# Optimization experiments

Measured on AMD Instinct MI355X. Metric: run time of the kernel, lower is better.

Reference implementation:

```python
import jax, jax.numpy as jnp
import numpy as np

H = 128          # hidden_size
GRID = 4         # grid_dim
CELL = 0.5       # cell_size
PRED_LEN = 12
EMB = H // 4     # social pooling embed dim = 32


def setup_inputs() -> dict:
    key = jax.random.key(0)
    ks = jax.random.split(key, 13)
    B, N, T = 16384, 64, 8
    s = 0.05
    return {
        "obs": jax.random.normal(ks[0], (B, T, 2), jnp.float32),
        "neighbors": jax.random.normal(ks[1], (B, N, T, 2), jnp.float32),
        "embed_table": jax.random.normal(ks[2], (GRID * GRID + 1, EMB), jnp.float32) * s,
        "W_in": jax.random.normal(ks[3], (H, 2), jnp.float32) * s,
        "b_in": jax.random.normal(ks[4], (H,), jnp.float32) * s,
        "W_sp": jax.random.normal(ks[5], (H, EMB), jnp.float32) * s,
        "b_sp": jax.random.normal(ks[6], (H,), jnp.float32) * s,
        "W_ih": jax.random.normal(ks[7], (4 * H, 2 * H), jnp.float32) * s,
        "W_hh": jax.random.normal(ks[8], (4 * H, H), jnp.float32) * s,
        "b_ih": jax.random.normal(ks[9], (4 * H,), jnp.float32) * s,
        "b_hh": jax.random.normal(ks[10], (4 * H,), jnp.float32) * s,
        "W_out": jax.random.normal(ks[11], (2, H), jnp.float32) * s,
        "b_out": jax.random.normal(ks[12], (2,), jnp.float32) * s,
    }


def reference(obs, neighbors, embed_table, W_in, b_in, W_sp, b_sp,
              W_ih, W_hh, b_ih, b_hh, W_out, b_out):
    B = obs.shape[0]
    half = GRID // 2

    def pool(rel):  # rel: [B, N, 2] -> [B, EMB]
        idx = jnp.clip(jnp.floor(rel / CELL).astype(jnp.int32), -half, half - 1) + half
        # after clamp+shift, idx in [0, GRID-1], so index is always valid (matches torch path)
        flat = idx[..., 0] * GRID + idx[..., 1]  # [B, N]
        return embed_table[flat].sum(axis=1)     # sum-pool over neighbors

    def lstm(h, c, x):  # torch LSTMCell gate order: i, f, g, o
        gates = x @ W_ih.T + b_ih + h @ W_hh.T + b_hh  # [B, 4H]
        i, f, g, o = jnp.split(gates, 4, axis=-1)
        c2 = jax.nn.sigmoid(f) * c + jax.nn.sigmoid(i) * jnp.tanh(g)
        h2 = jax.nn.sigmoid(o) * jnp.tanh(c2)
        return h2, c2

    def obs_step(carry, xs):
        h, c = carry
        o_t, nb_t = xs  # [B,2], [B,N,2]
        agent = o_t @ W_in.T + b_in                        # [B,H]
        social = pool(nb_t - o_t[:, None, :]) @ W_sp.T + b_sp  # [B,H]
        h, c = lstm(h, c, jnp.concatenate([agent, social], axis=-1))
        return (h, c), None

    h0 = jnp.zeros((B, H), obs.dtype)
    c0 = jnp.zeros((B, H), obs.dtype)
    obs_tf = jnp.swapaxes(obs, 0, 1)          # [T,B,2]
    nb_tf = jnp.moveaxis(neighbors, 2, 0)     # [T,B,N,2]
    (h, c), _ = jax.lax.scan(obs_step, (h0, c0), (obs_tf, nb_tf))

    def pred_step(carry, _):
        h, c, prev = carry
        agent = prev @ W_in.T + b_in
        x = jnp.concatenate([agent, jnp.zeros_like(agent)], axis=-1)
        h, c = lstm(h, c, x)
        disp = h @ W_out.T + b_out  # [B,2]
        return (h, c, disp), disp

    prev0 = jnp.zeros((B, 2), obs.dtype)
    _, fut = jax.lax.scan(pred_step, (h, c, prev0), None, length=PRED_LEN)
    return jnp.swapaxes(fut, 0, 1)  # [B, PRED_LEN, 2]
```

## Files before the change

kernel.cpp:

```cpp
#include <hip/hip_runtime.h>
#include <math.h>

typedef _Float16 f16;
typedef f16 f16x8 __attribute__((ext_vector_type(8)));
typedef float f32x4 __attribute__((ext_vector_type(4)));

#define Bsz   16384
#define Tobs  8
#define PREDL 12
#define MR    32

__device__ __forceinline__ float fast_sigm(float x) {
  float e = __builtin_amdgcn_exp2f(-1.44269504f * x);
  return __builtin_amdgcn_rcpf(1.f + e);
}
__device__ __forceinline__ float fast_tanh(float x) {
  float e = __builtin_amdgcn_exp2f(2.88539008f * x);
  return 1.f - 2.f * __builtin_amdgcn_rcpf(1.f + e);
}

#define AB(buf, kt, mt, lane, j) (((((buf)*4 + (kt))*2 + (mt))*64 + (lane))*8 + (j))
#define CA(t, mt, lane, j) ((((t)*2 + (mt))*64 + (lane))*8 + (j))

#define WF(ktw, w, nt, lane) ((size_t)((((ktw)*8 + (w))*4 + (nt))*64 + (lane)) * 8)

__global__ __launch_bounds__(64) void pack_all(
    const float* __restrict__ W_ih, const float* __restrict__ W_hh,
    const float* __restrict__ W_in, const float* __restrict__ W_sp,
    const float* __restrict__ table,
    const float* __restrict__ b_in, const float* __restrict__ b_sp,
    const float* __restrict__ b_ih, const float* __restrict__ b_hh,
    const float* __restrict__ W_out, const float* __restrict__ b_out,
    f16* __restrict__ Wfrag, float* __restrict__ biasO,
    float* __restrict__ biasP, float* __restrict__ biasPE) {
  const int blk = blockIdx.x;
  const int nt = blk >> 7, w = (blk >> 4) & 7, l = blk & 15;
  const int jo = nt * 128 + w * 16 + l;
  const int m = threadIdx.x;
  __shared__ float st[256];
  __shared__ float wspPS[32];
  __shared__ float cellsS[16];

  float a0 = W_ih[jo * 256 + m],        a1 = W_ih[jo * 256 + 64 + m];
  float s0 = W_ih[jo * 256 + 128 + m],  s1 = W_ih[jo * 256 + 192 + m];
  float hh0 = W_hh[jo * 128 + m],       hh1 = W_hh[jo * 128 + 64 + m];
  float bi0 = b_in[m], bi1 = b_in[64 + m];
  float bs0 = b_sp[m], bs1 = b_sp[64 + m];
  float wi00 = W_in[m * 2 + 0],        wi01 = W_in[m * 2 + 1];
  float wi10 = W_in[(64 + m) * 2 + 0], wi11 = W_in[(64 + m) * 2 + 1];
  float wo00 = W_out[m],       wo01 = W_out[64 + m];
  float wo10 = W_out[128 + m], wo11 = W_out[192 + m];

  auto red = [](float v) {
#pragma unroll
    for (int s = 1; s < 64; s <<= 1) v += __shfl_xor(v, s);
    return v;
  };

#pragma unroll 4
  for (int e = 0; e < 32; ++e) {
    float wp = red(s0 * W_sp[m * 32 + e] + s1 * W_sp[(64 + m) * 32 + e]);
    if (m == e) wspPS[e] = wp;
  }
  __syncthreads();
  if (m < 16) {
    float s = 0.f;
#pragma unroll
    for (int e = 0; e < 32; ++e) s += table[m * 32 + e] * wspPS[e];
    cellsS[m] = s;
  }

  float wio0 = red(a0 * wi00 + a1 * wi10);
  float wio1 = red(a0 * wi01 + a1 * wi11);
  float dotA = red(a0 * bi0 + a1 * bi1);
  float dotS = red(s0 * bs0 + s1 * bs1);

  st[m] = hh0;
  st[64 + m] = hh1;
  st[128 + m] = hh0 + wio0 * wo00 + wio1 * wo10;
  st[192 + m] = hh1 + wio0 * wo01 + wio1 * wo11;
  __syncthreads();

  if (m < 32) {
    int u = m & 15, kt = u >> 2, q = u & 3;
    int which = m >> 4;
    int ktw = which ? kt + 5 : kt;
    f16x8 v;
#pragma unroll
    for (int j = 0; j < 8; ++j) v[j] = (f16)st[which * 128 + kt * 32 + q * 8 + j];
    *(f16x8*)(Wfrag + WF(ktw, w, nt, q * 16 + l)) = v;
  } else if (m < 36) {
    int q = m - 32;
    f16x8 v;
#pragma unroll
    for (int j = 0; j < 8; ++j) {
      int kk = q * 8 + j;
      float x = (kk < 16) ? cellsS[kk] : (kk == 16 ? wio0 : (kk == 17 ? wio1 : 0.f));
      v[j] = (f16)x;
    }
    *(f16x8*)(Wfrag + WF(4, w, nt, q * 16 + l)) = v;
  } else if (m == 36) {
    int col = w * 64 + nt * 16 + l;
    float base = b_ih[jo] + b_hh[jo];
    biasO[col] = base + dotA + dotS;
    float bp = base + dotA;
    biasP[col] = bp;
    biasPE[col] = bp + wio0 * b_out[0] + wio1 * b_out[1];
  }
}

__global__ __launch_bounds__(512, 2) void social_lstm_main(
    const float* __restrict__ obs, const float* __restrict__ nb,
    const f16* __restrict__ Wfrag, const float* __restrict__ biasO,
    const float* __restrict__ biasP, const float* __restrict__ biasPE,
    const float* __restrict__ W_out, const float* __restrict__ b_out,
    float* __restrict__ out) {
  __shared__ __align__(16) f16 Abuf[2 * 4 * 2 * 64 * 8];
  __shared__ __align__(16) f16 cntA[8 * 2 * 64 * 8];

  const int tid = threadIdx.x;
  const int w = tid >> 6, ln = tid & 63;
  const int q = ln >> 4, l = ln & 15;
  const int b0 = blockIdx.x * MR;

  for (int i = tid; i < 2048; i += 512) ((uint32_t*)Abuf)[i] = 0u;
  for (int i = tid; i < 4096; i += 512) ((uint32_t*)cntA)[i] = 0u;
  __syncthreads();

  {
    const int g = ln >> 4, lg = ln & 15;
    const int r = w * 4 + g;
    const float4* orow = (const float4*)(obs + (size_t)(b0 + r) * 16);
    float4 O0 = orow[0], O1 = orow[1], O2 = orow[2], O3 = orow[3];
    float ox[8] = {O0.x, O0.z, O1.x, O1.z, O2.x, O2.z, O3.x, O3.z};
    float oy[8] = {O0.y, O0.w, O1.y, O1.w, O2.y, O2.w, O3.y, O3.w};
    unsigned long long h[8] = {0ull, 0ull, 0ull, 0ull, 0ull, 0ull, 0ull, 0ull};
#pragma unroll
    for (int jt = 0; jt < 4; ++jt) {
      const float4* tr =
          (const float4*)(nb + ((size_t)(b0 + r) * 64 + (lg + 16 * jt)) * 16);
      float4 N0 = tr[0], N1 = tr[1], N2 = tr[2], N3 = tr[3];
      float nx[8] = {N0.x, N0.z, N1.x, N1.z, N2.x, N2.z, N3.x, N3.z};
      float ny[8] = {N0.y, N0.w, N1.y, N1.w, N2.y, N2.w, N3.y, N3.w};
#pragma unroll
      for (int t = 0; t < 8; ++t) {
        float rx = nx[t] - ox[t], ry = ny[t] - oy[t];
        int ix = (int)floorf(rx + rx);
        int iy = (int)floorf(ry + ry);
        ix = min(max(ix, -2), 1);
        iy = min(max(iy, -2), 1);
        int flat = (ix + 2) * 4 + (iy + 2);
        h[t] += 1ull << (flat * 4);
      }
    }
    auto shx = [](unsigned long long x, int msk) {
      unsigned lo = __shfl_xor((unsigned)x, msk);
      unsigned hi = __shfl_xor((unsigned)(x >> 32), msk);
      return ((unsigned long long)hi << 32) | lo;
    };
#pragma unroll
    for (int t = 0; t < 8; ++t) {
      unsigned long long v = h[t];
      v += shx(v, 1);
      unsigned long long e0 = v & 0x0F0F0F0F0F0F0F0Full;
      unsigned long long e1 = (v >> 4) & 0x0F0F0F0F0F0F0F0Full;
      e0 += shx(e0, 2); e1 += shx(e1, 2);
      e0 += shx(e0, 4); e1 += shx(e1, 4);
      e0 += shx(e0, 8); e1 += shx(e1, 8);
      unsigned long long wsel = (lg & 1) ? e1 : e0;
      unsigned cnt = (unsigned)(wsel >> ((lg >> 1) * 8)) & 0xFFu;
      cntA[CA(t, r >> 4, (lg >> 3) * 16 + (r & 15), lg & 7)] = (f16)(float)cnt;
    }
    int rr = tid >> 4, tt = (tid >> 1) & 7, comp = tid & 1;
    float xv = obs[(size_t)(b0 + rr) * 16 + tt * 2 + comp];
    cntA[CA(tt, rr >> 4, 2 * 16 + (rr & 15), comp)] = (f16)xv;
  }
  __builtin_amdgcn_sched_barrier(0);

  f16x8 Bh[4][4];
#pragma unroll
  for (int kt = 0; kt < 4; ++kt)
#pragma unroll
    for (int nt = 0; nt < 4; ++nt)
      Bh[kt][nt] = *(const f16x8*)(Wfrag + WF(kt, w, nt, ln));
  f16x8 Bx[4];
#pragma unroll
  for (int nt = 0; nt < 4; ++nt) Bx[nt] = *(const f16x8*)(Wfrag + WF(4, w, nt, ln));

  float creg[8];
#pragma unroll
  for (int i = 0; i < 8; ++i) creg[i] = 0.f;

  float bOr[4], bPr[4];
#pragma unroll
  for (int g2 = 0; g2 < 4; ++g2) {
    bOr[g2] = biasO[w * 64 + g2 * 16 + l];
    bPr[g2] = biasP[w * 64 + g2 * 16 + l];
  }

  const int hc = w * 16 + l;
  const int aw_kt = hc >> 5, aw_quad = (hc >> 3) & 3, aw_j = l & 7;

  f32x4 acc[2][4];

  auto acc_init = [&](const float* bq) {
#pragma unroll
    for (int mt = 0; mt < 2; ++mt)
#pragma unroll
      for (int nt = 0; nt < 4; ++nt)
        acc[mt][nt] = (f32x4){bq[nt], bq[nt], bq[nt], bq[nt]};
  };

  auto gemm_h = [&](int rb) {
#pragma unroll
    for (int kt = 0; kt < 4; ++kt) {
      f16x8 Af[2];
#pragma unroll
      for (int mt = 0; mt < 2; ++mt) Af[mt] = *(const f16x8*)(&Abuf[AB(rb, kt, mt, ln, 0)]);
#pragma unroll
      for (int mt = 0; mt < 2; ++mt)
#pragma unroll
        for (int nt = 0; nt < 4; ++nt)
          acc[mt][nt] =
              __builtin_amdgcn_mfma_f32_16x16x32_f16(Af[mt], Bh[kt][nt], acc[mt][nt], 0, 0, 0);
    }
  };

  auto epilogue = [&](int wbuf) {
#pragma unroll
    for (int mt = 0; mt < 2; ++mt) {
#pragma unroll
      for (int reg = 0; reg < 4; ++reg) {
        float p0 = acc[mt][0][reg];
        float p1 = acc[mt][1][reg];
        float p2 = acc[mt][2][reg];
        float p3 = acc[mt][3][reg];
        float iv = fast_sigm(p0), fv = fast_sigm(p1);
        float gv = fast_tanh(p2), ov = fast_sigm(p3);
        int ci = mt * 4 + reg;
        float c2 = fv * creg[ci] + iv * gv;
        creg[ci] = c2;
        float hv = ov * fast_tanh(c2);
        Abuf[AB(wbuf, aw_kt, mt, (q * 4 + reg) + 16 * aw_quad, aw_j)] = (f16)hv;
      }
    }
  };

#pragma unroll
  for (int t = 0; t < Tobs; ++t) {
    const int rb = t & 1, wb = rb ^ 1;
    __syncthreads();
    f16x8 Ax[2];
#pragma unroll
    for (int mt = 0; mt < 2; ++mt) Ax[mt] = *(const f16x8*)(&cntA[CA(t, mt, ln, 0)]);
    acc_init(bOr);
#pragma unroll
    for (int mt = 0; mt < 2; ++mt)
#pragma unroll
      for (int nt = 0; nt < 4; ++nt)
        acc[mt][nt] = __builtin_amdgcn_mfma_f32_16x16x32_f16(Ax[mt], Bx[nt], acc[mt][nt], 0, 0, 0);
    gemm_h(rb);
    epilogue(wb);
  }

  {
    const int rb = Tobs & 1, wb = rb ^ 1;
    __syncthreads();
    acc_init(bPr);
    gemm_h(rb);
    epilogue(wb);
  }

#pragma unroll
  for (int kt = 0; kt < 4; ++kt)
#pragma unroll
    for (int nt = 0; nt < 4; ++nt)
      Bh[kt][nt] = *(const f16x8*)(Wfrag + WF(kt + 5, w, nt, ln));
  float bEr[4];
#pragma unroll
  for (int g2 = 0; g2 < 4; ++g2) bEr[g2] = biasPE[w * 64 + g2 * 16 + l];

  const int d_oi = tid >> 3, d_seg = tid & 7;
  const int d_row = d_oi >> 1, d_jj = d_oi & 1;
  const int d_kt = d_seg >> 1, d_q0 = (d_seg & 1) * 2;
  float wor[16];
  {
    const float4* wp = (const float4*)(W_out + d_jj * 128 + d_seg * 16);
#pragma unroll
    for (int u = 0; u < 4; ++u) {
      float4 v = wp[u];
      wor[4 * u] = v.x; wor[4 * u + 1] = v.y; wor[4 * u + 2] = v.z; wor[4 * u + 3] = v.w;
    }
  }
  const float d_bo = b_out[d_jj];

  auto disp_out = [&](int rbuf, int p) {
    f16x8 hA = *(const f16x8*)(&Abuf[AB(rbuf, d_kt, d_row >> 4, (d_row & 15) + 16 * d_q0, 0)]);
    f16x8 hB = *(const f16x8*)(&Abuf[AB(rbuf, d_kt, d_row >> 4, (d_row & 15) + 16 * (d_q0 + 1), 0)]);
    float s = 0.f;
#pragma unroll
    for (int u = 0; u < 8; ++u) s += wor[u] * (float)hA[u];
#pragma unroll
    for (int u = 0; u < 8; ++u) s += wor[8 + u] * (float)hB[u];
    s += __shfl_xor(s, 1);
    s += __shfl_xor(s, 2);
    s += __shfl_xor(s, 4);
    if ((tid & 7) == 0)
      out[((size_t)(b0 + d_row)) * (PREDL * 2) + p * 2 + d_jj] = s + d_bo;
  };

  for (int p = 1; p < PREDL; ++p) {
    const int s = Tobs + p;
    const int rb = s & 1, wb = rb ^ 1;
    __syncthreads();
    disp_out(rb, p - 1);
    acc_init(bEr);
    gemm_h(rb);
    epilogue(wb);
  }
  __syncthreads();
  disp_out((Tobs + PREDL) & 1, PREDL - 1);
}

extern "C" void kernel_launch(void* const* d_in, const int* in_sizes, int n_in,
                              void* d_out, int out_size, void* d_ws, size_t ws_size,
                              hipStream_t stream) {
  const float* obs   = (const float*)d_in[0];
  const float* nbrs  = (const float*)d_in[1];
  const float* table = (const float*)d_in[2];
  const float* W_in  = (const float*)d_in[3];
  const float* b_in  = (const float*)d_in[4];
  const float* W_sp  = (const float*)d_in[5];
  const float* b_sp  = (const float*)d_in[6];
  const float* W_ih  = (const float*)d_in[7];
  const float* W_hh  = (const float*)d_in[8];
  const float* b_ih  = (const float*)d_in[9];
  const float* b_hh  = (const float*)d_in[10];
  const float* W_out = (const float*)d_in[11];
  const float* b_out = (const float*)d_in[12];
  float* out = (float*)d_out;

  char* ws = (char*)d_ws;
  f16*   Wfrag  = (f16*)(ws);
  float* biasO  = (float*)(ws + 294912);
  float* biasP  = (float*)(ws + 296960);
  float* biasPE = (float*)(ws + 299008);

  pack_all<<<512, 64, 0, stream>>>(W_ih, W_hh, W_in, W_sp, table, b_in, b_sp, b_ih, b_hh,
                                   W_out, b_out, Wfrag, biasO, biasP, biasPE);
  social_lstm_main<<<Bsz / MR, 512, 0, stream>>>(obs, nbrs, Wfrag, biasO, biasP, biasPE,
                                                 W_out, b_out, out);
}
```

Measured before the change: 205.7 us.

## Split LSTM step into per-M-tile halves and raise occupancy to four blocks per CU

The launch-bounds hint goes from two to four 512-thread blocks per CU. To fit that register budget, each recurrent step is split into two half-steps, one per 16-row M tile, so only four accumulators are live instead of eight. The prediction bias load is moved later, the neighbor loads are all issued up front into a register array to expose memory parallelism, and the sched_barrier is removed. Higher occupancy should hide MFMA and LDS latency, at the risk of spills under the tighter register cap and less ILP within each wave.

```diff
diff --git a/kernel.cpp b/kernel.cpp
--- a/kernel.cpp
+++ b/kernel.cpp
@@ -109,7 +109,7 @@
   }
 }
 
-__global__ __launch_bounds__(512, 2) void social_lstm_main(
+__global__ __launch_bounds__(512, 4) void social_lstm_main(
     const float* __restrict__ obs, const float* __restrict__ nb,
     const f16* __restrict__ Wfrag, const float* __restrict__ biasO,
     const float* __restrict__ biasP, const float* __restrict__ biasPE,
@@ -130,6 +130,14 @@
   {
     const int g = ln >> 4, lg = ln & 15;
     const int r = w * 4 + g;
+    float4 T[16];
+#pragma unroll
+    for (int jt = 0; jt < 4; ++jt) {
+      const float4* tr =
+          (const float4*)(nb + ((size_t)(b0 + r) * 64 + (lg + 16 * jt)) * 16);
+#pragma unroll
+      for (int u = 0; u < 4; ++u) T[jt * 4 + u] = tr[u];
+    }
     const float4* orow = (const float4*)(obs + (size_t)(b0 + r) * 16);
     float4 O0 = orow[0], O1 = orow[1], O2 = orow[2], O3 = orow[3];
     float ox[8] = {O0.x, O0.z, O1.x, O1.z, O2.x, O2.z, O3.x, O3.z};
@@ -137,11 +145,10 @@
     unsigned long long h[8] = {0ull, 0ull, 0ull, 0ull, 0ull, 0ull, 0ull, 0ull};
 #pragma unroll
     for (int jt = 0; jt < 4; ++jt) {
-      const float4* tr =
-          (const float4*)(nb + ((size_t)(b0 + r) * 64 + (lg + 16 * jt)) * 16);
-      float4 N0 = tr[0], N1 = tr[1], N2 = tr[2], N3 = tr[3];
-      float nx[8] = {N0.x, N0.z, N1.x, N1.z, N2.x, N2.z, N3.x, N3.z};
-      float ny[8] = {N0.y, N0.w, N1.y, N1.w, N2.y, N2.w, N3.y, N3.w};
+      float nx[8] = {T[jt*4+0].x, T[jt*4+0].z, T[jt*4+1].x, T[jt*4+1].z,
+                     T[jt*4+2].x, T[jt*4+2].z, T[jt*4+3].x, T[jt*4+3].z};
+      float ny[8] = {T[jt*4+0].y, T[jt*4+0].w, T[jt*4+1].y, T[jt*4+1].w,
+                     T[jt*4+2].y, T[jt*4+2].w, T[jt*4+3].y, T[jt*4+3].w};
 #pragma unroll
       for (int t = 0; t < 8; ++t) {
         float rx = nx[t] - ox[t], ry = ny[t] - oy[t];
@@ -175,7 +182,6 @@
     float xv = obs[(size_t)(b0 + rr) * 16 + tt * 2 + comp];
     cntA[CA(tt, rr >> 4, 2 * 16 + (rr & 15), comp)] = (f16)xv;
   }
-  __builtin_amdgcn_sched_barrier(0);
 
   f16x8 Bh[4][4];
 #pragma unroll
@@ -191,58 +197,40 @@
 #pragma unroll
   for (int i = 0; i < 8; ++i) creg[i] = 0.f;
 
-  float bOr[4], bPr[4];
-#pragma unroll
-  for (int g2 = 0; g2 < 4; ++g2) {
-    bOr[g2] = biasO[w * 64 + g2 * 16 + l];
-    bPr[g2] = biasP[w * 64 + g2 * 16 + l];
-  }
+  float bOr[4];
+#pragma unroll
+  for (int g2 = 0; g2 < 4; ++g2) bOr[g2] = biasO[w * 64 + g2 * 16 + l];
 
   const int hc = w * 16 + l;
   const int aw_kt = hc >> 5, aw_quad = (hc >> 3) & 3, aw_j = l & 7;
 
-  f32x4 acc[2][4];
-
-  auto acc_init = [&](const float* bq) {
-#pragma unroll
-    for (int mt = 0; mt < 2; ++mt)
+  auto step_half = [&](int rb, int wb, int mt, const float* bq, bool ex, int t) {
+    f32x4 a[4];
+#pragma unroll
+    for (int nt = 0; nt < 4; ++nt) a[nt] = (f32x4){bq[nt], bq[nt], bq[nt], bq[nt]};
+    if (ex) {
+      f16x8 Ax = *(const f16x8*)(&cntA[CA(t, mt, ln, 0)]);
 #pragma unroll
       for (int nt = 0; nt < 4; ++nt)
-        acc[mt][nt] = (f32x4){bq[nt], bq[nt], bq[nt], bq[nt]};
-  };
-
-  auto gemm_h = [&](int rb) {
+        a[nt] = __builtin_amdgcn_mfma_f32_16x16x32_f16(Ax, Bx[nt], a[nt], 0, 0, 0);
+    }
 #pragma unroll
     for (int kt = 0; kt < 4; ++kt) {
-      f16x8 Af[2];
-#pragma unroll
-      for (int mt = 0; mt < 2; ++mt) Af[mt] = *(const f16x8*)(&Abuf[AB(rb, kt, mt, ln, 0)]);
-#pragma unroll
-      for (int mt = 0; mt < 2; ++mt)
-#pragma unroll
-        for (int nt = 0; nt < 4; ++nt)
-          acc[mt][nt] =
-              __builtin_amdgcn_mfma_f32_16x16x32_f16(Af[mt], Bh[kt][nt], acc[mt][nt], 0, 0, 0);
-    }
-  };
-
-  auto epilogue = [&](int wbuf) {
-#pragma unroll
-    for (int mt = 0; mt < 2; ++mt) {
-#pragma unroll
-      for (int reg = 0; reg < 4; ++reg) {
-        float p0 = acc[mt][0][reg];
-        float p1 = acc[mt][1][reg];
-        float p2 = acc[mt][2][reg];
-        float p3 = acc[mt][3][reg];
-        float iv = fast_sigm(p0), fv = fast_sigm(p1);
-        float gv = fast_tanh(p2), ov = fast_sigm(p3);
-        int ci = mt * 4 + reg;
-        float c2 = fv * creg[ci] + iv * gv;
-        creg[ci] = c2;
-        float hv = ov * fast_tanh(c2);
-        Abuf[AB(wbuf, aw_kt, mt, (q * 4 + reg) + 16 * aw_quad, aw_j)] = (f16)hv;
-      }
+      f16x8 Af = *(const f16x8*)(&Abuf[AB(rb, kt, mt, ln, 0)]);
+#pragma unroll
+      for (int nt = 0; nt < 4; ++nt)
+        a[nt] = __builtin_amdgcn_mfma_f32_16x16x32_f16(Af, Bh[kt][nt], a[nt], 0, 0, 0);
+    }
+#pragma unroll
+    for (int reg = 0; reg < 4; ++reg) {
+      float p0 = a[0][reg], p1 = a[1][reg], p2 = a[2][reg], p3 = a[3][reg];
+      float iv = fast_sigm(p0), fv = fast_sigm(p1);
+      float gv = fast_tanh(p2), ov = fast_sigm(p3);
+      int ci = mt * 4 + reg;
+      float c2 = fv * creg[ci] + iv * gv;
+      creg[ci] = c2;
+      float hv = ov * fast_tanh(c2);
+      Abuf[AB(wb, aw_kt, mt, (q * 4 + reg) + 16 * aw_quad, aw_j)] = (f16)hv;
     }
   };
 
@@ -250,25 +238,18 @@
   for (int t = 0; t < Tobs; ++t) {
     const int rb = t & 1, wb = rb ^ 1;
     __syncthreads();
-    f16x8 Ax[2];
-#pragma unroll
-    for (int mt = 0; mt < 2; ++mt) Ax[mt] = *(const f16x8*)(&cntA[CA(t, mt, ln, 0)]);
-    acc_init(bOr);
-#pragma unroll
-    for (int mt = 0; mt < 2; ++mt)
-#pragma unroll
-      for (int nt = 0; nt < 4; ++nt)
-        acc[mt][nt] = __builtin_amdgcn_mfma_f32_16x16x32_f16(Ax[mt], Bx[nt], acc[mt][nt], 0, 0, 0);
-    gemm_h(rb);
-    epilogue(wb);
+    step_half(rb, wb, 0, bOr, true, t);
+    step_half(rb, wb, 1, bOr, true, t);
   }
 
   {
+    float bPr[4];
+#pragma unroll
+    for (int g2 = 0; g2 < 4; ++g2) bPr[g2] = biasP[w * 64 + g2 * 16 + l];
     const int rb = Tobs & 1, wb = rb ^ 1;
     __syncthreads();
-    acc_init(bPr);
-    gemm_h(rb);
-    epilogue(wb);
+    step_half(rb, wb, 0, bPr, false, 0);
+    step_half(rb, wb, 1, bPr, false, 0);
   }
 
 #pragma unroll
@@ -314,9 +295,8 @@
     const int rb = s & 1, wb = rb ^ 1;
     __syncthreads();
     disp_out(rb, p - 1);
-    acc_init(bEr);
-    gemm_h(rb);
-    epilogue(wb);
+    step_half(rb, wb, 0, bEr, false, 0);
+    step_half(rb, wb, 1, bEr, false, 0);
   }
   __syncthreads();
   disp_out((Tobs + PREDL) & 1, PREDL - 1);
```

Result: slower. 400.5 us (+94.7%).
